# Kernel optimization log

Hardware: AMD Instinct MI355X
Metric: run time of the kernel (lower is better)

Reference implementation:

```python
import jax, jax.numpy as jnp
import numpy as np

GROUPS = 8
NUM_HEADS = 8
EPS = 1e-5


def setup_inputs() -> dict:
    key = jax.random.key(0)
    ks = jax.random.split(key, 3)
    C = 512
    x = jax.random.normal(ks[0], (2, C, 64, 64), dtype=jnp.float32)
    norm_w = jnp.ones((C,), jnp.float32)
    norm_b = jnp.zeros((C,), jnp.float32)
    qkv_w = jax.random.normal(ks[1], (3 * C, C), dtype=jnp.float32) * (C ** -0.5)
    qkv_b = jnp.zeros((3 * C,), jnp.float32)
    proj_w = jax.random.normal(ks[2], (C, C), dtype=jnp.float32) * (C ** -0.5)
    proj_b = jnp.zeros((C,), jnp.float32)
    return {"x": x, "norm_w": norm_w, "norm_b": norm_b,
            "qkv_w": qkv_w, "qkv_b": qkv_b,
            "proj_w": proj_w, "proj_b": proj_b}


def reference(x, norm_w, norm_b, qkv_w, qkv_b, proj_w, proj_b):
    b, c, h, w = x.shape
    n = h * w
    hd = c // NUM_HEADS

    # GroupNorm(8, c): normalize over (channels-in-group, h, w)
    xg = x.reshape(b, GROUPS, c // GROUPS, h, w)
    mean = jnp.mean(xg, axis=(2, 3, 4), keepdims=True)
    var = jnp.var(xg, axis=(2, 3, 4), keepdims=True)
    xg = (xg - mean) * jax.lax.rsqrt(var + EPS)
    x_norm = xg.reshape(b, c, h, w) * norm_w[None, :, None, None] + norm_b[None, :, None, None]

    x_flat = x_norm.reshape(b, c, n)  # (b, c, n)
    # 1x1 Conv1d == channel-wise linear
    qkv = jnp.einsum('oc,bcn->bon', qkv_w, x_flat) + qkv_b[None, :, None]
    q, k, v = jnp.split(qkv, 3, axis=1)
    q = q.reshape(b, NUM_HEADS, hd, n)
    k = k.reshape(b, NUM_HEADS, hd, n)
    v = v.reshape(b, NUM_HEADS, hd, n)

    attn = jnp.einsum('bhdn,bhdm->bhnm', q, k) * (hd ** -0.5)  # (b,h,n,n)
    attn = jax.nn.softmax(attn, axis=-1)
    out = jnp.einsum('bhnm,bhdm->bhdn', attn, v).reshape(b, c, n)

    out = jnp.einsum('oc,bcn->bon', proj_w, out) + proj_b[None, :, None]
    return x + out.reshape(b, c, h, w)
```

## Files before the change

kernel.cpp:

```cpp
#include <hip/hip_runtime.h>
#include <stdint.h>

#define B_   2
#define C_   512
#define N_   4096
#define G_   8
#define NH_  8
#define HD_  64
#define GRPELEMS ((C_ / G_) * N_)
#define NCHUNK 16

typedef __bf16 bf16x8 __attribute__((ext_vector_type(8)));
typedef float  f32x4  __attribute__((ext_vector_type(4)));

#if __has_builtin(__builtin_amdgcn_exp2f)
#define EXP2(x) __builtin_amdgcn_exp2f(x)
#else
#define EXP2(x) exp2f(x)
#endif

__device__ inline unsigned f2bf(float f) {
    union { float f; unsigned u; } v; v.f = f;
    return (v.u + 0x7FFFu + ((v.u >> 16) & 1u)) >> 16;
}
__device__ inline __bf16 tobf(float f) {
    unsigned short u = (unsigned short)f2bf(f);
    union { unsigned short u; __bf16 b; } c; c.u = u;
    return c.b;
}
__device__ inline unsigned pktrunc(float f0, float f1) {
    return __builtin_amdgcn_perm(__float_as_uint(f1), __float_as_uint(f0),
                                 0x07060302u);
}

#define GLOAD16(g, l)                                                     \
    __builtin_amdgcn_global_load_lds(                                     \
        (const __attribute__((address_space(1))) unsigned*)(g),           \
        (__attribute__((address_space(3))) unsigned*)(l), 16, 0, 0)

__global__ __launch_bounds__(256) void prep(const float* __restrict__ x,
                                            const float* __restrict__ qw,
                                            const float* __restrict__ pw,
                                            float* __restrict__ psum,
                                            float* __restrict__ psq,
                                            __bf16* __restrict__ dq,
                                            __bf16* __restrict__ dp) {
    const int blk = blockIdx.x;
    const int t = threadIdx.x;
    if (blk < 256) {
        const float4* p = (const float4*)x + (size_t)blk * 4096;
        float s = 0.f, s2 = 0.f;
#pragma unroll
        for (int i = 0; i < 16; ++i) {
            float4 v = p[t + (i << 8)];
            s  += v.x + v.y + v.z + v.w;
            s2 += v.x * v.x + v.y * v.y + v.z * v.z + v.w * v.w;
        }
#pragma unroll
        for (int off = 1; off < 64; off <<= 1) {
            s  += __shfl_xor(s, off);
            s2 += __shfl_xor(s2, off);
        }
        __shared__ float rs[4], rq[4];
        if ((t & 63) == 0) { rs[t >> 6] = s; rq[t >> 6] = s2; }
        __syncthreads();
        if (t == 0) {
            psum[blk] = rs[0] + rs[1] + rs[2] + rs[3];
            psq[blk]  = rq[0] + rq[1] + rq[2] + rq[3];
        }
    } else {
        const int QW4 = (3 * C_ * C_) / 4;
        int idx = (blk - 256) * 256 + t;
        float4 v; __bf16* dst; int o;
        if (idx < QW4) { v = ((const float4*)qw)[idx]; dst = dq; o = idx; }
        else           { v = ((const float4*)pw)[idx - QW4]; dst = dp; o = idx - QW4; }
        uint2 pk;
        pk.x = f2bf(v.x) | (f2bf(v.y) << 16);
        pk.y = f2bf(v.z) | (f2bf(v.w) << 16);
        *(uint2*)(dst + (size_t)o * 4) = pk;
    }
}

__global__ __launch_bounds__(256) void gn_apply_t(const float* __restrict__ x,
                                                  const float* __restrict__ w,
                                                  const float* __restrict__ bb,
                                                  const float* __restrict__ psum,
                                                  const float* __restrict__ psq,
                                                  __bf16* __restrict__ xnT) {
    const int p0 = blockIdx.x << 6, c0 = blockIdx.y << 6, b = blockIdx.z;
    __shared__ __bf16 T[64][76];
    __shared__ float red[2 * NCHUNK];
    __shared__ float smr[2];
    const int tid = threadIdx.x;
    const int bg = b * G_ + (c0 >> 6);

    if (tid < NCHUNK)            red[tid] = psum[bg * NCHUNK + tid];
    else if (tid < 2 * NCHUNK)   red[tid] = psq[bg * NCHUNK + tid - NCHUNK];
    __syncthreads();
    if (tid == 0) {
        float s = 0.f, q = 0.f;
#pragma unroll
        for (int i = 0; i < NCHUNK; ++i) { s += red[i]; q += red[NCHUNK + i]; }
        const float inv = 1.f / (float)GRPELEMS;
        float mean = s * inv;
        float var  = q * inv - mean * mean;
        smr[0] = mean;
        smr[1] = rsqrtf(var + 1e-5f);
    }
    __syncthreads();
    const float mean = smr[0], rstd = smr[1];

    const int tr  = tid >> 4;
    const int tc4 = (tid & 15) << 2;
    const float* xb = x + ((size_t)b * C_ + c0) * N_ + p0;
#pragma unroll
    for (int cc = tr; cc < 64; cc += 16) {
        int c = c0 + cc;
        float sc = rstd * w[c];
        float sh = bb[c] - mean * sc;
        float4 v = *(const float4*)(xb + (size_t)cc * N_ + tc4);
        T[tc4 + 0][cc] = tobf(v.x * sc + sh);
        T[tc4 + 1][cc] = tobf(v.y * sc + sh);
        T[tc4 + 2][cc] = tobf(v.z * sc + sh);
        T[tc4 + 3][cc] = tobf(v.w * sc + sh);
    }
    __syncthreads();
    __bf16* dst = xnT + ((size_t)b * N_ + p0) * C_ + c0;
#pragma unroll
    for (int pp = tr; pp < 64; pp += 16)
        *(uint2*)(dst + (size_t)pp * C_ + tc4) = *(const uint2*)&T[pp][tc4];
}

template <int M_TOTAL, int EPI>
__global__ __launch_bounds__(256) void gemm_bf16(const __bf16* __restrict__ A,
                                                 const __bf16* __restrict__ Bm,
                                                 const float* __restrict__ bias,
                                                 const float* __restrict__ resid,
                                                 __bf16* __restrict__ qT,
                                                 __bf16* __restrict__ kT,
                                                 __bf16* __restrict__ vB,
                                                 float* __restrict__ Y) {
    const int b  = blockIdx.z;
    const int M0 = blockIdx.y << 7;
    const int N0 = blockIdx.x << 7;
    const int tid = threadIdx.x;
    const int w = tid >> 6, lane = tid & 63;
    const int quad = lane >> 4, l16 = lane & 15;
    const int wr = w >> 1, wc = w & 1;

    __shared__ __bf16 As[128 * 64];
    __shared__ __bf16 Bs[128 * 64];

    const __bf16* Bb = Bm + (size_t)b * ((size_t)N_ * C_);

    const int srow = lane >> 3;
    const int sg   = lane & 7;

    f32x4 acc[4][4];
#pragma unroll
    for (int mt = 0; mt < 4; ++mt)
#pragma unroll
        for (int nt = 0; nt < 4; ++nt) acc[mt][nt] = (f32x4){0.f, 0.f, 0.f, 0.f};

    for (int k0 = 0; k0 < C_; k0 += 64) {
        __syncthreads();
#pragma unroll
        for (int i = 0; i < 4; ++i) {
            int r  = (w << 5) + (i << 3) + srow;
            int gc = ((sg ^ (r & 7)) << 3);
            const __bf16* ga = A  + (size_t)(M0 + r) * C_ + k0 + gc;
            const __bf16* gb = Bb + (size_t)(N0 + r) * C_ + k0 + gc;
            GLOAD16(ga, As + (((w << 2) + i) << 9));
            GLOAD16(gb, Bs + (((w << 2) + i) << 9));
        }
        __syncthreads();

#pragma unroll
        for (int kk = 0; kk < 2; ++kk) {
            bf16x8 af[4], bfr[4];
            const int gk = (kk << 2) + quad;
#pragma unroll
            for (int mt = 0; mt < 4; ++mt) {
                int m = (wr << 6) + (mt << 4) + l16;
                af[mt] = *(const bf16x8*)&As[(m << 6) + ((gk ^ (m & 7)) << 3)];
            }
#pragma unroll
            for (int nt = 0; nt < 4; ++nt) {
                int n = (wc << 6) + (nt << 4) + l16;
                bfr[nt] = *(const bf16x8*)&Bs[(n << 6) + ((gk ^ (n & 7)) << 3)];
            }
#pragma unroll
            for (int mt = 0; mt < 4; ++mt)
#pragma unroll
                for (int nt = 0; nt < 4; ++nt)
                    acc[mt][nt] = __builtin_amdgcn_mfma_f32_16x16x32_bf16(
                        af[mt], bfr[nt], acc[mt][nt], 0, 0, 0);
        }
    }

    if (EPI == 0) {
        const int t = M0 >> 9;
        const float sc = (t == 0) ? (0.125f * 1.44269504f) : 1.f;
#pragma unroll
        for (int mt = 0; mt < 4; ++mt) {
            const int o0 = M0 + (wr << 6) + (mt << 4) + (quad << 2);
            const int h  = (o0 >> 6) & 7;
            const int d0 = o0 & 63;
            const size_t bh = (size_t)b * NH_ + h;
            float bi[4];
#pragma unroll
            for (int r = 0; r < 4; ++r) bi[r] = bias[o0 + r];
            if (t < 2) {
                __bf16* dst = (t == 0 ? qT : kT) + (bh * N_) * HD_ + d0;
#pragma unroll
                for (int nt = 0; nt < 4; ++nt) {
                    int p = N0 + (wc << 6) + (nt << 4) + l16;
                    f32x4 v = acc[mt][nt];
                    uint2 pk;
                    pk.x = f2bf((v[0] + bi[0]) * sc) | (f2bf((v[1] + bi[1]) * sc) << 16);
                    pk.y = f2bf((v[2] + bi[2]) * sc) | (f2bf((v[3] + bi[3]) * sc) << 16);
                    *(uint2*)(dst + (size_t)p * HD_) = pk;
                }
            } else {
                __bf16* dst = vB + bh * ((size_t)HD_ * N_);
#pragma unroll
                for (int nt = 0; nt < 4; ++nt) {
                    int p = N0 + (wc << 6) + (nt << 4) + l16;
                    f32x4 v = acc[mt][nt];
#pragma unroll
                    for (int r = 0; r < 4; ++r)
                        dst[(size_t)(d0 + r) * N_ + p] = tobf(v[r] + bi[r]);
                }
            }
        }
    } else {
#pragma unroll
        for (int mt = 0; mt < 4; ++mt) {
            const int o0 = M0 + (wr << 6) + (mt << 4) + (quad << 2);
            float bi[4];
#pragma unroll
            for (int r = 0; r < 4; ++r) bi[r] = bias[o0 + r];
#pragma unroll
            for (int nt = 0; nt < 4; ++nt) {
                int p = N0 + (wc << 6) + (nt << 4) + l16;
                f32x4 v = acc[mt][nt];
#pragma unroll
                for (int r = 0; r < 4; ++r) {
                    size_t off = ((size_t)b * C_ + o0 + r) * N_ + p;
                    Y[off] = v[r] + bi[r] + resid[off];
                }
            }
        }
    }
}

__global__ __launch_bounds__(256) void attn_mfma(const __bf16* __restrict__ qT,
                                                 const __bf16* __restrict__ kT,
                                                 const __bf16* __restrict__ vB,
                                                 __bf16* __restrict__ attT) {
    const int tid  = threadIdx.x;
    const int w    = tid >> 6;
    const int lane = tid & 63;
    const int quad = lane >> 4;
    const int l16  = lane & 15;
    const int l7   = l16 & 7;
    const int h = blockIdx.y, b = blockIdx.z;
    const int qw0 = (blockIdx.x << 7) + (w << 5);

    __shared__ __bf16 Ks[2][64][64];
    __shared__ __bf16 Vs[2][80][64];
    __shared__ __bf16 Ps[4][32][64];

    const size_t bh = (size_t)b * NH_ + h;
    const __bf16* qTb = qT + bh * ((size_t)N_ * HD_);
    const __bf16* kTb = kT + bh * ((size_t)N_ * HD_);
    const __bf16* vBb = vB + bh * ((size_t)HD_ * N_);

    {
        int r = tid >> 3;
        int c = (tid & 7) << 3;
        __bf16 val = ((r & 15) == 0) ? (__bf16)1.0f : (__bf16)0.0f;
        __bf16* dst = &Vs[r >> 4][64 + (r & 15)][c];
#pragma unroll
        for (int u = 0; u < 8; ++u) dst[u] = val;
    }

    bf16x8 qf[2][2];
#pragma unroll
    for (int qt = 0; qt < 2; ++qt)
#pragma unroll
        for (int hh = 0; hh < 2; ++hh)
            qf[qt][hh] = *(const bf16x8*)(qTb +
                (size_t)(qw0 + (qt << 4) + l16) * HD_ + (hh << 5) + (quad << 3));

    const int rrel = lane >> 3;
    const int gsw  = ((lane & 7) ^ rrel) << 3;

    auto stage = [&](int it, int buf) {
        const int kb = it << 6;
#pragma unroll
        for (int c = 0; c < 2; ++c) {
            const int rb = (w << 4) + (c << 3);
            const __bf16* gk = kTb + (size_t)(kb + rb + rrel) * HD_ + gsw;
            GLOAD16(gk, &Ks[buf][rb][0]);
            const __bf16* gv = vBb + (size_t)(rb + rrel) * N_ + kb + gsw;
            GLOAD16(gv, &Vs[buf][rb][0]);
        }
    };

    const f32x4 zero4 = {0.f, 0.f, 0.f, 0.f};
    f32x4 o[5][2];
#pragma unroll
    for (int dt = 0; dt < 5; ++dt) { o[dt][0] = zero4; o[dt][1] = zero4; }

    stage(0, 0);

    for (int it = 0; it < 64; ++it) {
        const int cur = it & 1;
        __syncthreads();
        if (it < 63) stage(it + 1, cur ^ 1);

        f32x4 s[4][2];
#pragma unroll
        for (int kt = 0; kt < 4; ++kt) { s[kt][0] = zero4; s[kt][1] = zero4; }
#pragma unroll
        for (int hh = 0; hh < 2; ++hh) {
#pragma unroll
            for (int kt = 0; kt < 4; ++kt) {
                bf16x8 a = *(const bf16x8*)&Ks[cur][(kt << 4) + l16]
                                              [(((hh << 2) + quad) ^ l7) << 3];
                s[kt][0] = __builtin_amdgcn_mfma_f32_16x16x32_bf16(a, qf[0][hh], s[kt][0], 0, 0, 0);
                s[kt][1] = __builtin_amdgcn_mfma_f32_16x16x32_bf16(a, qf[1][hh], s[kt][1], 0, 0, 0);
            }
        }

#pragma unroll
        for (int qt = 0; qt < 2; ++qt)
#pragma unroll
            for (int kt = 0; kt < 4; ++kt) {
                f32x4 sv = s[kt][qt];
                float e0 = EXP2(sv[0]), e1 = EXP2(sv[1]);
                float e2 = EXP2(sv[2]), e3 = EXP2(sv[3]);
                uint2 pk;
                pk.x = pktrunc(e0, e1);
                pk.y = pktrunc(e2, e3);
                *(uint2*)&Ps[w][(qt << 4) + l16]
                            [(((kt << 2) + quad) ^ (l7 << 1)) << 2] = pk;
            }

#pragma unroll
        for (int hh = 0; hh < 2; ++hh) {
            bf16x8 pf0 = *(const bf16x8*)&Ps[w][l16]
                          [(((hh << 3) + (quad << 1)) ^ (l7 << 1)) << 2];
            bf16x8 pf1 = *(const bf16x8*)&Ps[w][16 + l16]
                          [(((hh << 3) + (quad << 1)) ^ (l7 << 1)) << 2];
#pragma unroll
            for (int dt = 0; dt < 5; ++dt) {
                bf16x8 a = *(const bf16x8*)&Vs[cur][(dt << 4) + l16]
                                              [(((hh << 2) + quad) ^ l7) << 3];
                o[dt][0] = __builtin_amdgcn_mfma_f32_16x16x32_bf16(a, pf0, o[dt][0], 0, 0, 0);
                o[dt][1] = __builtin_amdgcn_mfma_f32_16x16x32_bf16(a, pf1, o[dt][1], 0, 0, 0);
            }
        }
    }

    float lq[2];
    lq[0] = __shfl(o[4][0][0], l16, 64);
    lq[1] = __shfl(o[4][1][0], l16, 64);

#pragma unroll
    for (int qt = 0; qt < 2; ++qt) {
        float inv = 1.f / lq[qt];
        int n = qw0 + (qt << 4) + l16;
        __bf16* dst = attT + ((size_t)b * N_ + n) * C_ + h * HD_ + (quad << 2);
#pragma unroll
        for (int dt = 0; dt < 4; ++dt) {
            uint2 pk;
            pk.x = f2bf(o[dt][qt][0] * inv) | (f2bf(o[dt][qt][1] * inv) << 16);
            pk.y = f2bf(o[dt][qt][2] * inv) | (f2bf(o[dt][qt][3] * inv) << 16);
            *(uint2*)(dst + (dt << 4)) = pk;
        }
    }
}

extern "C" void kernel_launch(void* const* d_in, const int* in_sizes, int n_in,
                              void* d_out, int out_size, void* d_ws, size_t ws_size,
                              hipStream_t stream) {
    const float* x      = (const float*)d_in[0];
    const float* norm_w = (const float*)d_in[1];
    const float* norm_b = (const float*)d_in[2];
    const float* qkv_w  = (const float*)d_in[3];
    const float* qkv_b  = (const float*)d_in[4];
    const float* proj_w = (const float*)d_in[5];
    const float* proj_b = (const float*)d_in[6];
    float* out = (float*)d_out;

    const size_t BCN = (size_t)B_ * C_ * N_;
    float* psum  = (float*)d_ws;
    float* psq   = psum + 256;
    __bf16* xnT  = (__bf16*)(psq + 256);
    __bf16* qT   = xnT + BCN;
    __bf16* kT   = qT + BCN;
    __bf16* vB   = kT + BCN;
    __bf16* attT = vB + BCN;
    __bf16* wq   = attT + BCN;
    __bf16* wp   = wq + (size_t)3 * C_ * C_;

    prep<<<1280, 256, 0, stream>>>(x, qkv_w, proj_w, psum, psq, wq, wp);
    gn_apply_t<<<dim3(N_ / 64, C_ / 64, B_), 256, 0, stream>>>(
        x, norm_w, norm_b, psum, psq, xnT);
    gemm_bf16<3 * C_, 0><<<dim3(N_ / 128, 3 * C_ / 128, B_), 256, 0, stream>>>(
        wq, xnT, qkv_b, nullptr, qT, kT, vB, nullptr);
    attn_mfma<<<dim3(N_ / 128, NH_, B_), 256, 0, stream>>>(qT, kT, vB, attT);
    gemm_bf16<C_, 1><<<dim3(N_ / 128, C_ / 128, B_), 256, 0, stream>>>(
        wp, attT, proj_b, x, nullptr, nullptr, nullptr, out);
}
```

Before: 227.7 us.

## Pre-pack K and V in MFMA fragment layout and load directly to registers

The QKV GEMM epilogue now writes K and V in a packed layout where each lane's 8-element MFMA operand is contiguous. The attention kernel loads K and V fragments straight from global memory into registers, dropping the LDS staging, the async global-to-LDS copies and the per-iteration block barrier. The K fragments for the next tile are prefetched into registers. The softmax denominator, previously produced by an extra ones-row MFMA tile, is now summed in registers from the truncated exponentials and reduced with shuffles. This removes a fifth of the PV MFMAs and the LDS traffic, but each wave now fetches K/V itself from global memory or cache, with no sharing across the four waves, and V loads have less latency hiding.

```diff
diff --git a/kernel.cpp b/kernel.cpp
--- a/kernel.cpp
+++ b/kernel.cpp
@@ -31,6 +31,9 @@
 __device__ inline unsigned pktrunc(float f0, float f1) {
     return __builtin_amdgcn_perm(__float_as_uint(f1), __float_as_uint(f0),
                                  0x07060302u);
+}
+__device__ inline float trunc_bf(float f) {
+    return __uint_as_float(__float_as_uint(f) & 0xffff0000u);
 }
 
 #define GLOAD16(g, l)                                                     \
@@ -137,8 +140,8 @@
                                                  const float* __restrict__ bias,
                                                  const float* __restrict__ resid,
                                                  __bf16* __restrict__ qT,
-                                                 __bf16* __restrict__ kT,
-                                                 __bf16* __restrict__ vB,
+                                                 __bf16* __restrict__ kP,
+                                                 __bf16* __restrict__ vP,
                                                  float* __restrict__ Y) {
     const int b  = blockIdx.z;
     const int M0 = blockIdx.y << 7;
@@ -210,8 +213,8 @@
             float bi[4];
 #pragma unroll
             for (int r = 0; r < 4; ++r) bi[r] = bias[o0 + r];
-            if (t < 2) {
-                __bf16* dst = (t == 0 ? qT : kT) + (bh * N_) * HD_ + d0;
+            if (t == 0) {
+                __bf16* dst = qT + (bh * N_) * HD_ + d0;
 #pragma unroll
                 for (int nt = 0; nt < 4; ++nt) {
                     int p = N0 + (wc << 6) + (nt << 4) + l16;
@@ -221,15 +224,29 @@
                     pk.y = f2bf((v[2] + bi[2]) * sc) | (f2bf((v[3] + bi[3]) * sc) << 16);
                     *(uint2*)(dst + (size_t)p * HD_) = pk;
                 }
-            } else {
-                __bf16* dst = vB + bh * ((size_t)HD_ * N_);
+            } else if (t == 1) {
+                __bf16* dst = kP + bh * ((size_t)N_ * HD_);
+                const size_t kkbase = (size_t)(d0 >> 3) * N_;
+                const int rem = d0 & 7;
 #pragma unroll
                 for (int nt = 0; nt < 4; ++nt) {
                     int p = N0 + (wc << 6) + (nt << 4) + l16;
                     f32x4 v = acc[mt][nt];
+                    uint2 pk;
+                    pk.x = f2bf(v[0] + bi[0]) | (f2bf(v[1] + bi[1]) << 16);
+                    pk.y = f2bf(v[2] + bi[2]) | (f2bf(v[3] + bi[3]) << 16);
+                    *(uint2*)(dst + (kkbase + p) * 8 + rem) = pk;
+                }
+            } else {
+                __bf16* dst = vP + bh * ((size_t)HD_ * N_);
+#pragma unroll
+                for (int nt = 0; nt < 4; ++nt) {
+                    int p = N0 + (wc << 6) + (nt << 4) + l16;
+                    const size_t gb2 = ((size_t)(p >> 3) * HD_) * 8 + (p & 7);
+                    f32x4 v = acc[mt][nt];
 #pragma unroll
                     for (int r = 0; r < 4; ++r)
-                        dst[(size_t)(d0 + r) * N_ + p] = tobf(v[r] + bi[r]);
+                        dst[gb2 + (size_t)(d0 + r) * 8] = tobf(v[r] + bi[r]);
                 }
             }
         }
@@ -255,8 +272,8 @@
 }
 
 __global__ __launch_bounds__(256) void attn_mfma(const __bf16* __restrict__ qT,
-                                                 const __bf16* __restrict__ kT,
-                                                 const __bf16* __restrict__ vB,
+                                                 const __bf16* __restrict__ kP,
+                                                 const __bf16* __restrict__ vP,
                                                  __bf16* __restrict__ attT) {
     const int tid  = threadIdx.x;
     const int w    = tid >> 6;
@@ -267,23 +284,12 @@
     const int h = blockIdx.y, b = blockIdx.z;
     const int qw0 = (blockIdx.x << 7) + (w << 5);
 
-    __shared__ __bf16 Ks[2][64][64];
-    __shared__ __bf16 Vs[2][80][64];
     __shared__ __bf16 Ps[4][32][64];
 
     const size_t bh = (size_t)b * NH_ + h;
     const __bf16* qTb = qT + bh * ((size_t)N_ * HD_);
-    const __bf16* kTb = kT + bh * ((size_t)N_ * HD_);
-    const __bf16* vBb = vB + bh * ((size_t)HD_ * N_);
-
-    {
-        int r = tid >> 3;
-        int c = (tid & 7) << 3;
-        __bf16 val = ((r & 15) == 0) ? (__bf16)1.0f : (__bf16)0.0f;
-        __bf16* dst = &Vs[r >> 4][64 + (r & 15)][c];
-#pragma unroll
-        for (int u = 0; u < 8; ++u) dst[u] = val;
-    }
+    const __bf16* kPb = kP + bh * ((size_t)N_ * HD_);
+    const __bf16* vPb = vP + bh * ((size_t)HD_ * N_);
 
     bf16x8 qf[2][2];
 #pragma unroll
@@ -293,46 +299,44 @@
             qf[qt][hh] = *(const bf16x8*)(qTb +
                 (size_t)(qw0 + (qt << 4) + l16) * HD_ + (hh << 5) + (quad << 3));
 
-    const int rrel = lane >> 3;
-    const int gsw  = ((lane & 7) ^ rrel) << 3;
-
-    auto stage = [&](int it, int buf) {
+#define KADDR(hh, kt, kb) (kPb + (((size_t)((hh << 2) + quad) * N_) + (kb) + ((kt) << 4) + l16) * 8)
+#define VADDR(h2, dt, kb) (vPb + (((size_t)(((kb) >> 3) + ((h2) << 2) + quad) * HD_) + ((dt) << 4) + l16) * 8)
+
+    const f32x4 zero4 = {0.f, 0.f, 0.f, 0.f};
+    f32x4 o[4][2];
+#pragma unroll
+    for (int dt = 0; dt < 4; ++dt) { o[dt][0] = zero4; o[dt][1] = zero4; }
+    float lacc[2] = {0.f, 0.f};
+
+    bf16x8 kf[2][4];
+#pragma unroll
+    for (int hh = 0; hh < 2; ++hh)
+#pragma unroll
+        for (int kt = 0; kt < 4; ++kt)
+            kf[hh][kt] = *(const bf16x8*)KADDR(hh, kt, 0);
+
+    for (int it = 0; it < 64; ++it) {
         const int kb = it << 6;
-#pragma unroll
-        for (int c = 0; c < 2; ++c) {
-            const int rb = (w << 4) + (c << 3);
-            const __bf16* gk = kTb + (size_t)(kb + rb + rrel) * HD_ + gsw;
-            GLOAD16(gk, &Ks[buf][rb][0]);
-            const __bf16* gv = vBb + (size_t)(rb + rrel) * N_ + kb + gsw;
-            GLOAD16(gv, &Vs[buf][rb][0]);
-        }
-    };
-
-    const f32x4 zero4 = {0.f, 0.f, 0.f, 0.f};
-    f32x4 o[5][2];
-#pragma unroll
-    for (int dt = 0; dt < 5; ++dt) { o[dt][0] = zero4; o[dt][1] = zero4; }
-
-    stage(0, 0);
-
-    for (int it = 0; it < 64; ++it) {
-        const int cur = it & 1;
-        __syncthreads();
-        if (it < 63) stage(it + 1, cur ^ 1);
+
+        bf16x8 vf[2][4];
+#pragma unroll
+        for (int h2 = 0; h2 < 2; ++h2)
+#pragma unroll
+            for (int dt = 0; dt < 4; ++dt)
+                vf[h2][dt] = *(const bf16x8*)VADDR(h2, dt, kb);
 
         f32x4 s[4][2];
 #pragma unroll
         for (int kt = 0; kt < 4; ++kt) { s[kt][0] = zero4; s[kt][1] = zero4; }
 #pragma unroll
-        for (int hh = 0; hh < 2; ++hh) {
+        for (int hh = 0; hh < 2; ++hh)
 #pragma unroll
             for (int kt = 0; kt < 4; ++kt) {
-                bf16x8 a = *(const bf16x8*)&Ks[cur][(kt << 4) + l16]
-                                              [(((hh << 2) + quad) ^ l7) << 3];
-                s[kt][0] = __builtin_amdgcn_mfma_f32_16x16x32_bf16(a, qf[0][hh], s[kt][0], 0, 0, 0);
-                s[kt][1] = __builtin_amdgcn_mfma_f32_16x16x32_bf16(a, qf[1][hh], s[kt][1], 0, 0, 0);
-            }
-        }
+                s[kt][0] = __builtin_amdgcn_mfma_f32_16x16x32_bf16(
+                    kf[hh][kt], qf[0][hh], s[kt][0], 0, 0, 0);
+                s[kt][1] = __builtin_amdgcn_mfma_f32_16x16x32_bf16(
+                    kf[hh][kt], qf[1][hh], s[kt][1], 0, 0, 0);
+            }
 
 #pragma unroll
         for (int qt = 0; qt < 2; ++qt)
@@ -341,6 +345,8 @@
                 f32x4 sv = s[kt][qt];
                 float e0 = EXP2(sv[0]), e1 = EXP2(sv[1]);
                 float e2 = EXP2(sv[2]), e3 = EXP2(sv[3]);
+                lacc[qt] += (trunc_bf(e0) + trunc_bf(e1)) +
+                            (trunc_bf(e2) + trunc_bf(e3));
                 uint2 pk;
                 pk.x = pktrunc(e0, e1);
                 pk.y = pktrunc(e2, e3);
@@ -348,6 +354,14 @@
                             [(((kt << 2) + quad) ^ (l7 << 1)) << 2] = pk;
             }
 
+        if (it < 63) {
+#pragma unroll
+            for (int hh = 0; hh < 2; ++hh)
+#pragma unroll
+                for (int kt = 0; kt < 4; ++kt)
+                    kf[hh][kt] = *(const bf16x8*)KADDR(hh, kt, kb + 64);
+        }
+
 #pragma unroll
         for (int hh = 0; hh < 2; ++hh) {
             bf16x8 pf0 = *(const bf16x8*)&Ps[w][l16]
@@ -355,18 +369,23 @@
             bf16x8 pf1 = *(const bf16x8*)&Ps[w][16 + l16]
                           [(((hh << 3) + (quad << 1)) ^ (l7 << 1)) << 2];
 #pragma unroll
-            for (int dt = 0; dt < 5; ++dt) {
-                bf16x8 a = *(const bf16x8*)&Vs[cur][(dt << 4) + l16]
-                                              [(((hh << 2) + quad) ^ l7) << 3];
-                o[dt][0] = __builtin_amdgcn_mfma_f32_16x16x32_bf16(a, pf0, o[dt][0], 0, 0, 0);
-                o[dt][1] = __builtin_amdgcn_mfma_f32_16x16x32_bf16(a, pf1, o[dt][1], 0, 0, 0);
+            for (int dt = 0; dt < 4; ++dt) {
+                o[dt][0] = __builtin_amdgcn_mfma_f32_16x16x32_bf16(
+                    vf[hh][dt], pf0, o[dt][0], 0, 0, 0);
+                o[dt][1] = __builtin_amdgcn_mfma_f32_16x16x32_bf16(
+                    vf[hh][dt], pf1, o[dt][1], 0, 0, 0);
             }
         }
     }
 
     float lq[2];
-    lq[0] = __shfl(o[4][0][0], l16, 64);
-    lq[1] = __shfl(o[4][1][0], l16, 64);
+#pragma unroll
+    for (int qt = 0; qt < 2; ++qt) {
+        float v = lacc[qt];
+        v += __shfl_xor(v, 16);
+        v += __shfl_xor(v, 32);
+        lq[qt] = v;
+    }
 
 #pragma unroll
     for (int qt = 0; qt < 2; ++qt) {
@@ -381,6 +400,8 @@
             *(uint2*)(dst + (dt << 4)) = pk;
         }
     }
+#undef KADDR
+#undef VADDR
 }
 
 extern "C" void kernel_launch(void* const* d_in, const int* in_sizes, int n_in,
@@ -400,9 +421,9 @@
     float* psq   = psum + 256;
     __bf16* xnT  = (__bf16*)(psq + 256);
     __bf16* qT   = xnT + BCN;
-    __bf16* kT   = qT + BCN;
-    __bf16* vB   = kT + BCN;
-    __bf16* attT = vB + BCN;
+    __bf16* kP   = qT + BCN;
+    __bf16* vP   = kP + BCN;
+    __bf16* attT = vP + BCN;
     __bf16* wq   = attT + BCN;
     __bf16* wp   = wq + (size_t)3 * C_ * C_;
 
@@ -410,8 +431,8 @@
     gn_apply_t<<<dim3(N_ / 64, C_ / 64, B_), 256, 0, stream>>>(
         x, norm_w, norm_b, psum, psq, xnT);
     gemm_bf16<3 * C_, 0><<<dim3(N_ / 128, 3 * C_ / 128, B_), 256, 0, stream>>>(
-        wq, xnT, qkv_b, nullptr, qT, kT, vB, nullptr);
-    attn_mfma<<<dim3(N_ / 128, NH_, B_), 256, 0, stream>>>(qT, kT, vB, attT);
+        wq, xnT, qkv_b, nullptr, qT, kP, vP, nullptr);
+    attn_mfma<<<dim3(N_ / 128, NH_, B_), 256, 0, stream>>>(qT, kP, vP, attT);
     gemm_bf16<C_, 1><<<dim3(N_ / 128, C_ / 128, B_), 256, 0, stream>>>(
         wp, attT, proj_b, x, nullptr, nullptr, nullptr, out);
 }
```

After: 215.9 us. 1.05x faster.
